# Kernel optimization log

Measured on AMD Instinct MI355X. Metric: run time of the kernel, lower is better.

Reference implementation:

```python
import jax, jax.numpy as jnp
import numpy as np

N = 50000      # nodes (B-rep faces)
E = 800000     # directed edges (avg degree 16)
F_IN = 9       # 8 surface-type flags + is_feature
H1, H2, C = 512, 128, 2


def setup_inputs() -> dict:
    key = jax.random.key(0)
    ks = jax.random.split(key, 8)
    x = jax.random.normal(ks[0], (N, F_IN), dtype=jnp.float32)
    edge_index = jax.random.randint(ks[1], (2, E), 0, N, dtype=jnp.int64)
    W1 = jax.random.normal(ks[2], (F_IN, H1), dtype=jnp.float32) / np.sqrt(F_IN)
    b1 = jnp.zeros((H1,), dtype=jnp.float32)
    W2 = jax.random.normal(ks[3], (H1, H2), dtype=jnp.float32) / np.sqrt(H1)
    b2 = jnp.zeros((H2,), dtype=jnp.float32)
    W3 = jax.random.normal(ks[4], (H2, C), dtype=jnp.float32) / np.sqrt(H2)
    b3 = jnp.zeros((C,), dtype=jnp.float32)
    return {"x": x, "W1": W1, "b1": b1, "W2": W2, "b2": b2,
            "W3": W3, "b3": b3, "edge_index": edge_index}


def reference(x, W1, b1, W2, b2, W3, b3, edge_index):
    n = x.shape[0]
    self_idx = jnp.arange(n, dtype=edge_index.dtype)
    # GCN with self-loops and symmetric normalization (PyG gcn_norm)
    src = jnp.concatenate([edge_index[0], self_idx])  # [E+N]
    dst = jnp.concatenate([edge_index[1], self_idx])  # [E+N]
    deg = jax.ops.segment_sum(jnp.ones_like(src, dtype=x.dtype), dst, num_segments=n)
    dinv = jnp.where(deg > 0, jax.lax.rsqrt(jnp.maximum(deg, 1.0)), 0.0)
    norm = dinv[src] * dinv[dst]  # [E+N]

    def gcn(h, W, b):
        h = h @ W                                   # [N, out]
        msg = h[src] * norm[:, None]                # gather + scale
        return jax.ops.segment_sum(msg, dst, num_segments=n) + b  # scatter-add

    h = jax.nn.relu(gcn(x, W1, b1))
    h = jax.nn.relu(gcn(h, W2, b2))
    # F.dropout with training=False is identity (inference mode)
    h = gcn(h, W3, b3)
    return jax.nn.log_softmax(h, axis=1)
```

## Files before the change

### kernel.cpp

```cpp
#include <hip/hip_runtime.h>
#include <hip/hip_bf16.h>

typedef __attribute__((ext_vector_type(8))) short short8;
typedef __attribute__((ext_vector_type(4))) float float4v;
typedef unsigned int uint;

#define NBLK 192

static __device__ __forceinline__ float2 up_bf2(uint v) {
    float2 r;
    r.x = __uint_as_float(v << 16);
    r.y = __uint_as_float(v & 0xffff0000u);
    return r;
}
static __device__ __forceinline__ short f2bf_bits(float x) {
    union { __hip_bfloat16 h; short s; } u;
    u.h = __float2bfloat16(x);
    return u.s;
}


__global__ __launch_bounds__(256) void k_hist(const int* __restrict__ dst, int E, int chunk,
        int shift, int nbuck, int* __restrict__ histBlk) {
    __shared__ int h[256];
    h[threadIdx.x] = 0;
    __syncthreads();
    int blk = blockIdx.x;
    int e0 = blk * chunk, e1 = min(E, e0 + chunk);
    for (int e = e0 + threadIdx.x; e < e1; e += 256)
        atomicAdd(&h[dst[e] >> shift], 1);
    __syncthreads();
    if (threadIdx.x < nbuck) histBlk[threadIdx.x * NBLK + blk] = h[threadIdx.x];
}


__global__ __launch_bounds__(256) void k_btot(const int* __restrict__ histBlk,
                                              int* __restrict__ btot) {
    __shared__ int s[256];
    int b = blockIdx.x, t = threadIdx.x;
    s[t] = (t < NBLK) ? histBlk[b * NBLK + t] : 0;
    __syncthreads();
    for (int off = 128; off; off >>= 1) {
        if (t < off) s[t] += s[t + off];
        __syncthreads();
    }
    if (t == 0) btot[b] = s[0];
}


__global__ __launch_bounds__(256) void k_bscan(const int* __restrict__ histBlk,
        const int* __restrict__ btot, int nbuck,
        int* __restrict__ baseBlk, int* __restrict__ bucketBase) {
    __shared__ int s[256], sb[256];
    int b = blockIdx.x, t = threadIdx.x;
    int v = (t < NBLK) ? histBlk[b * NBLK + t] : 0;
    s[t] = v;
    sb[t] = (t < nbuck) ? btot[t] : 0;
    __syncthreads();
    for (int off = 1; off < 256; off <<= 1) {
        int u = (t >= off) ? s[t - off] : 0;
        int u2 = (t >= off) ? sb[t - off] : 0;
        __syncthreads();
        s[t] += u;
        sb[t] += u2;
        __syncthreads();
    }
    int base = (b > 0) ? sb[b - 1] : 0;
    if (t < NBLK) baseBlk[b * NBLK + t] = base + s[t] - v;
    if (t == 0) bucketBase[b] = base;
}


__global__ __launch_bounds__(256) void k_scatterbin(const int* __restrict__ src,
        const int* __restrict__ dst, int E, int chunk, int shift, int nbuck,
        const int* __restrict__ baseBlk, uint* __restrict__ binned) {
    __shared__ int cur[256];
    int blk = blockIdx.x;
    if (threadIdx.x < nbuck) cur[threadIdx.x] = baseBlk[threadIdx.x * NBLK + blk];
    __syncthreads();
    int e0 = blk * chunk, e1 = min(E, e0 + chunk);
    int mask = (1 << shift) - 1;
    for (int e = e0 + threadIdx.x; e < e1; e += 256) {
        int d = dst[e];
        int pos = atomicAdd(&cur[d >> shift], 1);
        binned[pos] = (uint)src[e] | ((uint)(d & mask) << 24);
    }
}


__global__ __launch_bounds__(256) void k_csrbuild(const uint* __restrict__ binned,
        const int* __restrict__ bucketBase, const float* __restrict__ x,
        int E, int shift, int n, int nbuck,
        int* __restrict__ row_ptr, float* __restrict__ dinv, float* __restrict__ xs,
        int* __restrict__ csr) {
    __shared__ int cnt[256], lcur[256];
    int b = blockIdx.x, t = threadIdx.x;
    cnt[t] = 0;
    __syncthreads();
    int lo = bucketBase[b];
    int hi = (b + 1 < nbuck) ? bucketBase[b + 1] : E;
    for (int e = lo + t; e < hi; e += 256)
        atomicAdd(&cnt[binned[e] >> 24], 1);
    __syncthreads();
    int c = cnt[t];
    lcur[t] = c;
    __syncthreads();
    for (int off = 1; off < 256; off <<= 1) {
        int u = (t >= off) ? lcur[t - off] : 0;
        __syncthreads();
        lcur[t] += u;
        __syncthreads();
    }
    int node0 = b << shift;
    int nodeEnd = min(n, (b + 1) << shift);
    int cntNodes = nodeEnd - node0;
    int myBase = lo + lcur[t] - c;
    if (t < cntNodes) {
        row_ptr[node0 + t] = myBase;
        dinv[node0 + t] = rsqrtf((float)(c + 1));
    }
    if (b == nbuck - 1 && t == 0) row_ptr[n] = E;
    for (int j = t; j < cntNodes * 9; j += 256) {
        int nl = j / 9, f = j - nl * 9;
        float dnl = rsqrtf((float)(cnt[nl] + 1));
        xs[(size_t)(node0 + nl) * 9 + f] = dnl * x[(size_t)(node0 + nl) * 9 + f];
    }
    __syncthreads();
    lcur[t] = myBase;
    __syncthreads();
    for (int e = lo + t; e < hi; e += 256) {
        uint p = binned[e];
        int pos = atomicAdd(&lcur[p >> 24], 1);
        csr[pos] = (int)(p & 0xFFFFFF);
    }
}


__global__ __launch_bounds__(256) void k_agg1w(const float* __restrict__ xs,
                       const float* __restrict__ dinv,
                       const int* __restrict__ row_ptr, const int* __restrict__ csr,
                       const float* __restrict__ W1, const float* __restrict__ W2,
                       __hip_bfloat16* __restrict__ aggx_bf,
                       __hip_bfloat16* __restrict__ W1frag,
                       __hip_bfloat16* __restrict__ W2frag, int n, int nagg) {
    int bid = blockIdx.x;
    if (bid >= nagg) {
        int xb = bid - nagg;
        if (xb < 8) {
            int t = xb * 256 + threadIdx.x;
            if (t < 32 * 64) {
                int ctile = t >> 6, lane = t & 63;
                int col = ctile * 16 + (lane & 15);
                int k0 = (lane >> 4) * 8;
                short8 o;
#pragma unroll
                for (int j = 0; j < 8; ++j) {
                    int k = k0 + j;
                    o[j] = f2bf_bits(k < 9 ? W1[k * 512 + col] : 0.f);
                }
                *reinterpret_cast<short8*>(W1frag + (size_t)t * 8) = o;
            }
        } else {
            int t = (xb - 8) * 256 + threadIdx.x;
            if (t < 64 * 128) {
                int kb = t >> 7, c = t & 127;
                const float* wp = W2 + (size_t)(kb * 8) * 128 + c;
                short8 o;
#pragma unroll
                for (int j = 0; j < 8; ++j) o[j] = f2bf_bits(wp[j * 128]);
                *reinterpret_cast<short8*>(W2frag + (size_t)t * 8) = o;
            }
        }
        return;
    }
    int node = bid * 16 + (threadIdx.x >> 4);
    if (node >= n) return;
    int f = threadIdx.x & 15;
    bool act = f < 9;
    float acc = act ? xs[node * 9 + f] : 0.f;
    int e0 = row_ptr[node], e1 = row_ptr[node + 1];
    int e = e0;
    for (; e + 4 <= e1; e += 4) {
        int s0 = csr[e], s1 = csr[e + 1], s2 = csr[e + 2], s3 = csr[e + 3];
        float x0 = act ? xs[s0 * 9 + f] : 0.f;
        float x1 = act ? xs[s1 * 9 + f] : 0.f;
        float x2 = act ? xs[s2 * 9 + f] : 0.f;
        float x3 = act ? xs[s3 * 9 + f] : 0.f;
        acc += (x0 + x1) + (x2 + x3);
    }
    for (; e < e1; ++e) {
        int sA = csr[e];
        acc += act ? xs[sA * 9 + f] : 0.f;
    }
    float v = act ? dinv[node] * acc : 0.f;
    __hip_bfloat16* op = aggx_bf + (size_t)node * 32;
    union { __hip_bfloat16 h; short s; } u;
    u.h = __float2bfloat16(v);
    reinterpret_cast<short*>(op)[f] = u.s;
    reinterpret_cast<short*>(op)[16 + f] = 0;
}

__global__ __launch_bounds__(512, 2) void k_l12(const __hip_bfloat16* __restrict__ aggx_bf,
                       const __hip_bfloat16* __restrict__ W1frag,
                       const __hip_bfloat16* __restrict__ W2frag,
                       const float* __restrict__ b1,
                       const float* __restrict__ dinv,
                       __hip_bfloat16* __restrict__ t2, int n, int npair) {
    __shared__ short h1s[8][2][16][40];
    int t = threadIdx.x;
    int wid = t >> 6, lane = t & 63;
    int pair = blockIdx.x * 8 + wid;
    if (pair >= npair) return;
    int r = lane & 15, quad = lane >> 4;
    short (*hs0)[40] = h1s[wid][0];
    short (*hs1)[40] = h1s[wid][1];

    int m0 = pair << 5;
    short8 aagg0 = *reinterpret_cast<const short8*>(
        aggx_bf + (size_t)(m0 + r) * 32 + quad * 8);
    short8 aagg1 = *reinterpret_cast<const short8*>(
        aggx_bf + (size_t)(m0 + 16 + r) * 32 + quad * 8);

    float4v acc0[8], acc1[8];
#pragma unroll
    for (int cg = 0; cg < 8; ++cg) {
        acc0[cg] = (float4v){0, 0, 0, 0};
        acc1[cg] = (float4v){0, 0, 0, 0};
    }

    for (int kt = 0; kt < 16; ++kt) {
        short8 bf0 = *reinterpret_cast<const short8*>(
            W1frag + ((size_t)(2 * kt) * 64 + lane) * 8);
        short8 bf1 = *reinterpret_cast<const short8*>(
            W1frag + ((size_t)(2 * kt + 1) * 64 + lane) * 8);
        float4v c00 = __builtin_amdgcn_mfma_f32_16x16x32_bf16(
            aagg0, bf0, (float4v){0, 0, 0, 0}, 0, 0, 0);
        float4v c01 = __builtin_amdgcn_mfma_f32_16x16x32_bf16(
            aagg0, bf1, (float4v){0, 0, 0, 0}, 0, 0, 0);
        float4v c10 = __builtin_amdgcn_mfma_f32_16x16x32_bf16(
            aagg1, bf0, (float4v){0, 0, 0, 0}, 0, 0, 0);
        float4v c11 = __builtin_amdgcn_mfma_f32_16x16x32_bf16(
            aagg1, bf1, (float4v){0, 0, 0, 0}, 0, 0, 0);
        float bb0 = b1[kt * 32 + r];
        float bb1 = b1[kt * 32 + 16 + r];
        short8 bfr[8];
#pragma unroll
        for (int cg = 0; cg < 8; ++cg)
            bfr[cg] = *reinterpret_cast<const short8*>(
                W2frag + (size_t)(((kt * 4 + quad) * 128) + cg * 16 + r) * 8);
#pragma unroll
        for (int i = 0; i < 4; ++i) {
            int row = quad * 4 + i;
            hs0[row][r]      = f2bf_bits(fmaxf(c00[i] + bb0, 0.f));
            hs0[row][16 + r] = f2bf_bits(fmaxf(c01[i] + bb1, 0.f));
            hs1[row][r]      = f2bf_bits(fmaxf(c10[i] + bb0, 0.f));
            hs1[row][16 + r] = f2bf_bits(fmaxf(c11[i] + bb1, 0.f));
        }
        short8 am0 = *reinterpret_cast<const short8*>(&hs0[r][quad * 8]);
        short8 am1 = *reinterpret_cast<const short8*>(&hs1[r][quad * 8]);
#pragma unroll
        for (int cg = 0; cg < 8; ++cg) {
            acc0[cg] = __builtin_amdgcn_mfma_f32_16x16x32_bf16(am0, bfr[cg], acc0[cg], 0, 0, 0);
            acc1[cg] = __builtin_amdgcn_mfma_f32_16x16x32_bf16(am1, bfr[cg], acc1[cg], 0, 0, 0);
        }
    }

#pragma unroll
    for (int i = 0; i < 4; ++i) {
        int node0 = m0 + quad * 4 + i;
        if (node0 < n) {
            float di = dinv[node0];
            __hip_bfloat16* op = t2 + (size_t)node0 * 128 + r;
#pragma unroll
            for (int cg = 0; cg < 8; ++cg)
                op[cg * 16] = __float2bfloat16(di * acc0[cg][i]);
        }
        int node1 = m0 + 16 + quad * 4 + i;
        if (node1 < n) {
            float di = dinv[node1];
            __hip_bfloat16* op = t2 + (size_t)node1 * 128 + r;
#pragma unroll
            for (int cg = 0; cg < 8; ++cg)
                op[cg * 16] = __float2bfloat16(di * acc1[cg][i]);
        }
    }
}


__global__ __launch_bounds__(256) void k_agg2(const uint* __restrict__ t2u,
                       const float* __restrict__ dinv,
                       const int* __restrict__ row_ptr, const int* __restrict__ csr,
                       const float* __restrict__ b2, const float* __restrict__ W3,
                       float2* __restrict__ t3, int n) {
    int node = blockIdx.x * 4 + (threadIdx.x >> 6);
    if (node >= n) return;
    int lane = threadIdx.x & 63;
    int half = lane >> 5;
    int cl = lane & 31;
    const uint2* t2v = reinterpret_cast<const uint2*>(t2u);

    float a0 = 0.f, a1 = 0.f, a2 = 0.f, a3 = 0.f;
    if (half == 0) {
        uint2 sv = t2v[(size_t)node * 32 + cl];
        float2 pa = up_bf2(sv.x), pb = up_bf2(sv.y);
        a0 = pa.x; a1 = pa.y; a2 = pb.x; a3 = pb.y;
    }

    int e0 = row_ptr[node], e1 = row_ptr[node + 1];
    int eb = e0;
    for (; eb + 16 <= e1; eb += 16) {
        int si[8];
        uint2 ri[8];
#pragma unroll
        for (int j = 0; j < 8; ++j) si[j] = csr[eb + half + 2 * j];
#pragma unroll
        for (int j = 0; j < 8; ++j) ri[j] = t2v[(size_t)si[j] * 32 + cl];
#pragma unroll
        for (int j = 0; j < 8; ++j) {
            float2 qa = up_bf2(ri[j].x), qb = up_bf2(ri[j].y);
            a0 += qa.x; a1 += qa.y; a2 += qb.x; a3 += qb.y;
        }
    }
    for (; eb + 4 <= e1; eb += 4) {
        int s0 = csr[eb + half], s1 = csr[eb + half + 2];
        uint2 r0 = t2v[(size_t)s0 * 32 + cl];
        uint2 r1 = t2v[(size_t)s1 * 32 + cl];
        float2 qa = up_bf2(r0.x), qb = up_bf2(r0.y);
        float2 qc = up_bf2(r1.x), qd = up_bf2(r1.y);
        a0 += qa.x + qc.x; a1 += qa.y + qc.y;
        a2 += qb.x + qd.x; a3 += qb.y + qd.y;
    }
    for (int e = eb + half; e < e1; e += 2) {
        uint2 rv = t2v[(size_t)csr[e] * 32 + cl];
        float2 qa = up_bf2(rv.x), qb = up_bf2(rv.y);
        a0 += qa.x; a1 += qa.y; a2 += qb.x; a3 += qb.y;
    }

    a0 += __shfl_xor(a0, 32);
    a1 += __shfl_xor(a1, 32);
    a2 += __shfl_xor(a2, 32);
    a3 += __shfl_xor(a3, 32);

    float di = dinv[node];
    float4 bb = *reinterpret_cast<const float4*>(b2 + 4 * cl);
    float h0 = fmaxf(di * a0 + bb.x, 0.f);
    float h1v = fmaxf(di * a1 + bb.y, 0.f);
    float h2 = fmaxf(di * a2 + bb.z, 0.f);
    float h3 = fmaxf(di * a3 + bb.w, 0.f);
    float4 wlo = *reinterpret_cast<const float4*>(W3 + 8 * cl);
    float4 whi = *reinterpret_cast<const float4*>(W3 + 8 * cl + 4);
    float c0 = h0 * wlo.x + h1v * wlo.z + h2 * whi.x + h3 * whi.z;
    float c1 = h0 * wlo.y + h1v * wlo.w + h2 * whi.y + h3 * whi.w;
#pragma unroll
    for (int off = 16; off; off >>= 1) {
        c0 += __shfl_xor(c0, off);
        c1 += __shfl_xor(c1, off);
    }
    if (lane == 0) t3[node] = make_float2(di * c0, di * c1);
}


__global__ void k_agg3(const float2* __restrict__ t3, const float* __restrict__ dinv,
                       const int* __restrict__ row_ptr, const int* __restrict__ csr,
                       const float* __restrict__ b3, float2* __restrict__ outv, int n) {
    int node = blockIdx.x * blockDim.x + threadIdx.x;
    if (node >= n) return;
    float2 s = t3[node];
    float a0 = s.x, a1 = s.y;
    int e0 = row_ptr[node], e1 = row_ptr[node + 1];
    int e = e0;
    for (; e + 4 <= e1; e += 4) {
        int s0 = csr[e], s1 = csr[e + 1], s2 = csr[e + 2], s3 = csr[e + 3];
        float2 q0 = t3[s0], q1 = t3[s1], q2 = t3[s2], q3 = t3[s3];
        a0 += q0.x + q1.x + q2.x + q3.x;
        a1 += q0.y + q1.y + q2.y + q3.y;
    }
    for (; e < e1; ++e) {
        float2 q0 = t3[csr[e]];
        a0 += q0.x;
        a1 += q0.y;
    }
    float di = dinv[node];
    float z0 = di * a0 + b3[0];
    float z1 = di * a1 + b3[1];
    float m = fmaxf(z0, z1);
    float lse = m + logf(expf(z0 - m) + expf(z1 - m));
    outv[node] = make_float2(z0 - lse, z1 - lse);
}


extern "C" void kernel_launch(void* const* d_in, const int* in_sizes, int n_in,
                              void* d_out, int out_size, void* d_ws, size_t ws_size,
                              hipStream_t stream) {
    const float* x  = (const float*)d_in[0];
    const float* W1 = (const float*)d_in[1];
    const float* b1 = (const float*)d_in[2];
    const float* W2 = (const float*)d_in[3];
    const float* b2 = (const float*)d_in[4];
    const float* W3 = (const float*)d_in[5];
    const float* b3 = (const float*)d_in[6];
    const int* edges = (const int*)d_in[7];

    int n = in_sizes[0] / 9;
    int E = in_sizes[7] / 2;
    const int* src = edges;
    const int* dst = edges + E;

    char* p = (char*)d_ws;
    auto alloc = [&](size_t bytes) {
        char* q = p;
        p += (bytes + 511) & ~(size_t)511;
        return q;
    };
    float* dinv       = (float*)alloc((size_t)n * 4);
    int*   row_ptr    = (int*)alloc((size_t)(n + 1) * 4);
    int*   csr        = (int*)alloc((size_t)E * 4);
    int*   histBlk    = (int*)alloc((size_t)256 * NBLK * 4);
    int*   baseBlk    = (int*)alloc((size_t)256 * NBLK * 4);
    int*   btot       = (int*)alloc(256 * 4);
    int*   bucketBase = (int*)alloc(256 * 4);
    uint*  binned     = (uint*)alloc((size_t)E * 4);
    float* xs         = (float*)alloc((size_t)n * 9 * 4);
    __hip_bfloat16* aggx_bf = (__hip_bfloat16*)alloc((size_t)(n + 64) * 32 * 2);
    __hip_bfloat16* W1frag  = (__hip_bfloat16*)alloc((size_t)32 * 64 * 8 * 2);
    __hip_bfloat16* W2frag  = (__hip_bfloat16*)alloc((size_t)64 * 128 * 8 * 2);
    __hip_bfloat16* t2 = (__hip_bfloat16*)alloc((size_t)n * 128 * 2);
    float2* t3 = (float2*)alloc((size_t)n * 8);

    const int B = 256;
    int shift = 8;
    int nbuck = ((n - 1) >> shift) + 1;
    int chunk = (E + NBLK - 1) / NBLK;

    k_hist<<<NBLK, B, 0, stream>>>(dst, E, chunk, shift, nbuck, histBlk);
    k_btot<<<nbuck, B, 0, stream>>>(histBlk, btot);
    k_bscan<<<nbuck, B, 0, stream>>>(histBlk, btot, nbuck, baseBlk, bucketBase);
    k_scatterbin<<<NBLK, B, 0, stream>>>(src, dst, E, chunk, shift, nbuck, baseBlk, binned);
    k_csrbuild<<<nbuck, B, 0, stream>>>(binned, bucketBase, x, E, shift, n, nbuck,
                                        row_ptr, dinv, xs, csr);

    int nagg = (n + 15) / 16;
    k_agg1w<<<nagg + 40, B, 0, stream>>>(xs, dinv, row_ptr, csr, W1, W2,
                                         aggx_bf, W1frag, W2frag, n, nagg);

    int ntile = (n + 15) / 16;
    int npair = (ntile + 1) / 2;
    k_l12<<<(npair + 7) / 8, 512, 0, stream>>>(aggx_bf, W1frag, W2frag, b1, dinv, t2, n, npair);
    k_agg2<<<(n + 3) / 4, 256, 0, stream>>>((const uint*)t2, dinv, row_ptr, csr, b2, W3, t3, n);

    k_agg3<<<(n + B - 1) / B, B, 0, stream>>>(t3, dinv, row_ptr, csr, b3, (float2*)d_out, n);
}
```

Before: 196.3 us.

## Replace two-pass bucketed CSR build with global-atomic degree count and fill

Replaces the five-kernel bucket-sort CSR construction (histogram, bucket totals, scan, scatter to binned, per-bucket local sort) with a global atomic per-node degree count, a per-256-node scan, and a fill pass using global atomic cursors. The intermediate binned array and its second pass are removed, and the W1/W2 fragment prep moves into the degree kernel. This trades launches and memory passes for heavy global atomic traffic on random node addresses, and neighbor order within a row becomes nondeterministic. A memset is added to zero the degree and bucket arrays.

```diff
diff --git a/kernel.cpp b/kernel.cpp
--- a/kernel.cpp
+++ b/kernel.cpp
@@ -20,132 +20,13 @@
 }
 
 
-__global__ __launch_bounds__(256) void k_hist(const int* __restrict__ dst, int E, int chunk,
-        int shift, int nbuck, int* __restrict__ histBlk) {
-    __shared__ int h[256];
-    h[threadIdx.x] = 0;
-    __syncthreads();
+__global__ __launch_bounds__(256) void k_deg(const int* __restrict__ dst, int E, int chunk,
+        int nbuck, int nblk, int* __restrict__ deg, int* __restrict__ btot,
+        const float* __restrict__ W1, const float* __restrict__ W2,
+        __hip_bfloat16* __restrict__ W1frag, __hip_bfloat16* __restrict__ W2frag) {
     int blk = blockIdx.x;
-    int e0 = blk * chunk, e1 = min(E, e0 + chunk);
-    for (int e = e0 + threadIdx.x; e < e1; e += 256)
-        atomicAdd(&h[dst[e] >> shift], 1);
-    __syncthreads();
-    if (threadIdx.x < nbuck) histBlk[threadIdx.x * NBLK + blk] = h[threadIdx.x];
-}
-
-
-__global__ __launch_bounds__(256) void k_btot(const int* __restrict__ histBlk,
-                                              int* __restrict__ btot) {
-    __shared__ int s[256];
-    int b = blockIdx.x, t = threadIdx.x;
-    s[t] = (t < NBLK) ? histBlk[b * NBLK + t] : 0;
-    __syncthreads();
-    for (int off = 128; off; off >>= 1) {
-        if (t < off) s[t] += s[t + off];
-        __syncthreads();
-    }
-    if (t == 0) btot[b] = s[0];
-}
-
-
-__global__ __launch_bounds__(256) void k_bscan(const int* __restrict__ histBlk,
-        const int* __restrict__ btot, int nbuck,
-        int* __restrict__ baseBlk, int* __restrict__ bucketBase) {
-    __shared__ int s[256], sb[256];
-    int b = blockIdx.x, t = threadIdx.x;
-    int v = (t < NBLK) ? histBlk[b * NBLK + t] : 0;
-    s[t] = v;
-    sb[t] = (t < nbuck) ? btot[t] : 0;
-    __syncthreads();
-    for (int off = 1; off < 256; off <<= 1) {
-        int u = (t >= off) ? s[t - off] : 0;
-        int u2 = (t >= off) ? sb[t - off] : 0;
-        __syncthreads();
-        s[t] += u;
-        sb[t] += u2;
-        __syncthreads();
-    }
-    int base = (b > 0) ? sb[b - 1] : 0;
-    if (t < NBLK) baseBlk[b * NBLK + t] = base + s[t] - v;
-    if (t == 0) bucketBase[b] = base;
-}
-
-
-__global__ __launch_bounds__(256) void k_scatterbin(const int* __restrict__ src,
-        const int* __restrict__ dst, int E, int chunk, int shift, int nbuck,
-        const int* __restrict__ baseBlk, uint* __restrict__ binned) {
-    __shared__ int cur[256];
-    int blk = blockIdx.x;
-    if (threadIdx.x < nbuck) cur[threadIdx.x] = baseBlk[threadIdx.x * NBLK + blk];
-    __syncthreads();
-    int e0 = blk * chunk, e1 = min(E, e0 + chunk);
-    int mask = (1 << shift) - 1;
-    for (int e = e0 + threadIdx.x; e < e1; e += 256) {
-        int d = dst[e];
-        int pos = atomicAdd(&cur[d >> shift], 1);
-        binned[pos] = (uint)src[e] | ((uint)(d & mask) << 24);
-    }
-}
-
-
-__global__ __launch_bounds__(256) void k_csrbuild(const uint* __restrict__ binned,
-        const int* __restrict__ bucketBase, const float* __restrict__ x,
-        int E, int shift, int n, int nbuck,
-        int* __restrict__ row_ptr, float* __restrict__ dinv, float* __restrict__ xs,
-        int* __restrict__ csr) {
-    __shared__ int cnt[256], lcur[256];
-    int b = blockIdx.x, t = threadIdx.x;
-    cnt[t] = 0;
-    __syncthreads();
-    int lo = bucketBase[b];
-    int hi = (b + 1 < nbuck) ? bucketBase[b + 1] : E;
-    for (int e = lo + t; e < hi; e += 256)
-        atomicAdd(&cnt[binned[e] >> 24], 1);
-    __syncthreads();
-    int c = cnt[t];
-    lcur[t] = c;
-    __syncthreads();
-    for (int off = 1; off < 256; off <<= 1) {
-        int u = (t >= off) ? lcur[t - off] : 0;
-        __syncthreads();
-        lcur[t] += u;
-        __syncthreads();
-    }
-    int node0 = b << shift;
-    int nodeEnd = min(n, (b + 1) << shift);
-    int cntNodes = nodeEnd - node0;
-    int myBase = lo + lcur[t] - c;
-    if (t < cntNodes) {
-        row_ptr[node0 + t] = myBase;
-        dinv[node0 + t] = rsqrtf((float)(c + 1));
-    }
-    if (b == nbuck - 1 && t == 0) row_ptr[n] = E;
-    for (int j = t; j < cntNodes * 9; j += 256) {
-        int nl = j / 9, f = j - nl * 9;
-        float dnl = rsqrtf((float)(cnt[nl] + 1));
-        xs[(size_t)(node0 + nl) * 9 + f] = dnl * x[(size_t)(node0 + nl) * 9 + f];
-    }
-    __syncthreads();
-    lcur[t] = myBase;
-    __syncthreads();
-    for (int e = lo + t; e < hi; e += 256) {
-        uint p = binned[e];
-        int pos = atomicAdd(&lcur[p >> 24], 1);
-        csr[pos] = (int)(p & 0xFFFFFF);
-    }
-}
-
-
-__global__ __launch_bounds__(256) void k_agg1w(const float* __restrict__ xs,
-                       const float* __restrict__ dinv,
-                       const int* __restrict__ row_ptr, const int* __restrict__ csr,
-                       const float* __restrict__ W1, const float* __restrict__ W2,
-                       __hip_bfloat16* __restrict__ aggx_bf,
-                       __hip_bfloat16* __restrict__ W1frag,
-                       __hip_bfloat16* __restrict__ W2frag, int n, int nagg) {
-    int bid = blockIdx.x;
-    if (bid >= nagg) {
-        int xb = bid - nagg;
+    if (blk >= nblk) {
+        int xb = blk - nblk;
         if (xb < 8) {
             int t = xb * 256 + threadIdx.x;
             if (t < 32 * 64) {
@@ -173,7 +54,78 @@
         }
         return;
     }
-    int node = bid * 16 + (threadIdx.x >> 4);
+    __shared__ int h[256];
+    int t = threadIdx.x;
+    h[t] = 0;
+    __syncthreads();
+    int e0 = blk * chunk, e1 = min(E, e0 + chunk);
+    for (int e = e0 + t; e < e1; e += 256) {
+        int d = dst[e];
+        atomicAdd(&deg[d], 1);
+        atomicAdd(&h[d >> 8], 1);
+    }
+    __syncthreads();
+    if (t < nbuck && h[t]) atomicAdd(&btot[t], h[t]);
+}
+
+
+__global__ __launch_bounds__(256) void k_scan(const int* __restrict__ deg,
+        const int* __restrict__ btot, const float* __restrict__ x,
+        int E, int n, int nbuck,
+        int* __restrict__ row_ptr, int* __restrict__ rowcur,
+        float* __restrict__ dinv, float* __restrict__ xs) {
+    __shared__ int s[256], sb[256], cnt[256];
+    int b = blockIdx.x, t = threadIdx.x;
+    int node = (b << 8) + t;
+    int d = (node < n) ? deg[node] : 0;
+    cnt[t] = d;
+    s[t] = d;
+    sb[t] = (t < nbuck) ? btot[t] : 0;
+    __syncthreads();
+    for (int off = 1; off < 256; off <<= 1) {
+        int u = (t >= off) ? s[t - off] : 0;
+        int u2 = (t >= off) ? sb[t - off] : 0;
+        __syncthreads();
+        s[t] += u;
+        sb[t] += u2;
+        __syncthreads();
+    }
+    int base = (b > 0) ? sb[b - 1] : 0;
+    int myBase = base + s[t] - cnt[t];
+    if (node < n) {
+        row_ptr[node] = myBase;
+        rowcur[node] = myBase;
+        dinv[node] = rsqrtf((float)(d + 1));
+    }
+    if (b == nbuck - 1 && t == 0) row_ptr[n] = E;
+    int node0 = b << 8;
+    int cntNodes = min(n, (b + 1) << 8) - node0;
+    for (int j = t; j < cntNodes * 9; j += 256) {
+        int nl = j / 9, f = j - nl * 9;
+        float dnl = rsqrtf((float)(cnt[nl] + 1));
+        xs[(size_t)(node0 + nl) * 9 + f] = dnl * x[(size_t)(node0 + nl) * 9 + f];
+    }
+}
+
+
+__global__ __launch_bounds__(256) void k_fill(const int* __restrict__ src,
+        const int* __restrict__ dst, int E, int chunk,
+        int* __restrict__ rowcur, int* __restrict__ csr) {
+    int blk = blockIdx.x, t = threadIdx.x;
+    int e0 = blk * chunk, e1 = min(E, e0 + chunk);
+    for (int e = e0 + t; e < e1; e += 256) {
+        int d = dst[e];
+        int pos = atomicAdd(&rowcur[d], 1);
+        csr[pos] = src[e];
+    }
+}
+
+
+__global__ __launch_bounds__(256) void k_agg1(const float* __restrict__ xs,
+                       const float* __restrict__ dinv,
+                       const int* __restrict__ row_ptr, const int* __restrict__ csr,
+                       __hip_bfloat16* __restrict__ aggx_bf, int n) {
+    int node = blockIdx.x * 16 + (threadIdx.x >> 4);
     if (node >= n) return;
     int f = threadIdx.x & 15;
     bool act = f < 9;
@@ -414,12 +366,10 @@
     };
     float* dinv       = (float*)alloc((size_t)n * 4);
     int*   row_ptr    = (int*)alloc((size_t)(n + 1) * 4);
+    int*   rowcur     = (int*)alloc((size_t)n * 4);
     int*   csr        = (int*)alloc((size_t)E * 4);
-    int*   histBlk    = (int*)alloc((size_t)256 * NBLK * 4);
-    int*   baseBlk    = (int*)alloc((size_t)256 * NBLK * 4);
-    int*   btot       = (int*)alloc(256 * 4);
-    int*   bucketBase = (int*)alloc(256 * 4);
-    uint*  binned     = (uint*)alloc((size_t)E * 4);
+    int*   deg        = (int*)alloc((size_t)(n + 256) * 4);
+    int*   btot       = deg + n;
     float* xs         = (float*)alloc((size_t)n * 9 * 4);
     __hip_bfloat16* aggx_bf = (__hip_bfloat16*)alloc((size_t)(n + 64) * 32 * 2);
     __hip_bfloat16* W1frag  = (__hip_bfloat16*)alloc((size_t)32 * 64 * 8 * 2);
@@ -428,20 +378,17 @@
     float2* t3 = (float2*)alloc((size_t)n * 8);
 
     const int B = 256;
-    int shift = 8;
-    int nbuck = ((n - 1) >> shift) + 1;
+    int nbuck = ((n - 1) >> 8) + 1;
     int chunk = (E + NBLK - 1) / NBLK;
 
-    k_hist<<<NBLK, B, 0, stream>>>(dst, E, chunk, shift, nbuck, histBlk);
-    k_btot<<<nbuck, B, 0, stream>>>(histBlk, btot);
-    k_bscan<<<nbuck, B, 0, stream>>>(histBlk, btot, nbuck, baseBlk, bucketBase);
-    k_scatterbin<<<NBLK, B, 0, stream>>>(src, dst, E, chunk, shift, nbuck, baseBlk, binned);
-    k_csrbuild<<<nbuck, B, 0, stream>>>(binned, bucketBase, x, E, shift, n, nbuck,
-                                        row_ptr, dinv, xs, csr);
-
-    int nagg = (n + 15) / 16;
-    k_agg1w<<<nagg + 40, B, 0, stream>>>(xs, dinv, row_ptr, csr, W1, W2,
-                                         aggx_bf, W1frag, W2frag, n, nagg);
+    hipMemsetAsync(deg, 0, (size_t)(n + 256) * 4, stream);
+    k_deg<<<NBLK + 40, B, 0, stream>>>(dst, E, chunk, nbuck, NBLK,
+                                       deg, btot, W1, W2, W1frag, W2frag);
+    k_scan<<<nbuck, B, 0, stream>>>(deg, btot, x, E, n, nbuck,
+                                    row_ptr, rowcur, dinv, xs);
+    k_fill<<<NBLK, B, 0, stream>>>(src, dst, E, chunk, rowcur, csr);
+
+    k_agg1<<<(n + 15) / 16, B, 0, stream>>>(xs, dinv, row_ptr, csr, aggx_bf, n);
 
     int ntile = (n + 15) / 16;
     int npair = (ntile + 1) / 2;
```

Result: slower. 243.4 us (+24.0%).

## Split layer-2 aggregation into feature slices with atomic reduction of layer-3 projection

Applied to the files above, without the earlier changes.

Replaces the per-node wavefront aggregation with a kernel where each block handles one of eight 16-feature slices for 32 nodes. Eight threads per node each gather a 4-byte bf16 pair per neighbor, so blocks working on the same slice touch a narrower band of the t2 table, which is meant to improve cache locality. Partial W3 projections from each slice are combined with float atomics into t3, which is now zeroed with a memset beforehand. In exchange, the CSR indices are re-read eight times, each gather is narrower, and the output costs extra atomics.

```diff
diff --git a/kernel.cpp b/kernel.cpp
--- a/kernel.cpp
+++ b/kernel.cpp
@@ -200,6 +200,7 @@
     reinterpret_cast<short*>(op)[16 + f] = 0;
 }
 
+
 __global__ __launch_bounds__(512, 2) void k_l12(const __hip_bfloat16* __restrict__ aggx_bf,
                        const __hip_bfloat16* __restrict__ W1frag,
                        const __hip_bfloat16* __restrict__ W2frag,
@@ -287,76 +288,59 @@
 }
 
 
-__global__ __launch_bounds__(256) void k_agg2(const uint* __restrict__ t2u,
+__global__ __launch_bounds__(256) void k_agg2s(const uint* __restrict__ t2u,
                        const float* __restrict__ dinv,
                        const int* __restrict__ row_ptr, const int* __restrict__ csr,
                        const float* __restrict__ b2, const float* __restrict__ W3,
                        float2* __restrict__ t3, int n) {
-    int node = blockIdx.x * 4 + (threadIdx.x >> 6);
+    int slice = blockIdx.x & 7;
+    int chunk = blockIdx.x >> 3;
+    int t = threadIdx.x;
+    int node = chunk * 32 + (t >> 3);
     if (node >= n) return;
-    int lane = threadIdx.x & 63;
-    int half = lane >> 5;
-    int cl = lane & 31;
-    const uint2* t2v = reinterpret_cast<const uint2*>(t2u);
-
-    float a0 = 0.f, a1 = 0.f, a2 = 0.f, a3 = 0.f;
-    if (half == 0) {
-        uint2 sv = t2v[(size_t)node * 32 + cl];
-        float2 pa = up_bf2(sv.x), pb = up_bf2(sv.y);
-        a0 = pa.x; a1 = pa.y; a2 = pb.x; a3 = pb.y;
-    }
+    int sub = t & 7;
+    int off = slice * 8 + sub;
+
+    float2 p0 = up_bf2(t2u[(size_t)node * 64 + off]);
+    float a0 = p0.x, a1 = p0.y;
 
     int e0 = row_ptr[node], e1 = row_ptr[node + 1];
-    int eb = e0;
-    for (; eb + 16 <= e1; eb += 16) {
+    int e = e0;
+    for (; e + 8 <= e1; e += 8) {
         int si[8];
-        uint2 ri[8];
-#pragma unroll
-        for (int j = 0; j < 8; ++j) si[j] = csr[eb + half + 2 * j];
-#pragma unroll
-        for (int j = 0; j < 8; ++j) ri[j] = t2v[(size_t)si[j] * 32 + cl];
+        uint ri[8];
+#pragma unroll
+        for (int j = 0; j < 8; ++j) si[j] = csr[e + j];
+#pragma unroll
+        for (int j = 0; j < 8; ++j) ri[j] = t2u[(size_t)si[j] * 64 + off];
 #pragma unroll
         for (int j = 0; j < 8; ++j) {
-            float2 qa = up_bf2(ri[j].x), qb = up_bf2(ri[j].y);
-            a0 += qa.x; a1 += qa.y; a2 += qb.x; a3 += qb.y;
-        }
-    }
-    for (; eb + 4 <= e1; eb += 4) {
-        int s0 = csr[eb + half], s1 = csr[eb + half + 2];
-        uint2 r0 = t2v[(size_t)s0 * 32 + cl];
-        uint2 r1 = t2v[(size_t)s1 * 32 + cl];
-        float2 qa = up_bf2(r0.x), qb = up_bf2(r0.y);
-        float2 qc = up_bf2(r1.x), qd = up_bf2(r1.y);
-        a0 += qa.x + qc.x; a1 += qa.y + qc.y;
-        a2 += qb.x + qd.x; a3 += qb.y + qd.y;
-    }
-    for (int e = eb + half; e < e1; e += 2) {
-        uint2 rv = t2v[(size_t)csr[e] * 32 + cl];
-        float2 qa = up_bf2(rv.x), qb = up_bf2(rv.y);
-        a0 += qa.x; a1 += qa.y; a2 += qb.x; a3 += qb.y;
-    }
-
-    a0 += __shfl_xor(a0, 32);
-    a1 += __shfl_xor(a1, 32);
-    a2 += __shfl_xor(a2, 32);
-    a3 += __shfl_xor(a3, 32);
+            float2 q = up_bf2(ri[j]);
+            a0 += q.x;
+            a1 += q.y;
+        }
+    }
+    for (; e < e1; ++e) {
+        float2 q = up_bf2(t2u[(size_t)csr[e] * 64 + off]);
+        a0 += q.x;
+        a1 += q.y;
+    }
 
     float di = dinv[node];
-    float4 bb = *reinterpret_cast<const float4*>(b2 + 4 * cl);
+    int c = off * 2;
+    float2 bb = *reinterpret_cast<const float2*>(b2 + c);
     float h0 = fmaxf(di * a0 + bb.x, 0.f);
-    float h1v = fmaxf(di * a1 + bb.y, 0.f);
-    float h2 = fmaxf(di * a2 + bb.z, 0.f);
-    float h3 = fmaxf(di * a3 + bb.w, 0.f);
-    float4 wlo = *reinterpret_cast<const float4*>(W3 + 8 * cl);
-    float4 whi = *reinterpret_cast<const float4*>(W3 + 8 * cl + 4);
-    float c0 = h0 * wlo.x + h1v * wlo.z + h2 * whi.x + h3 * whi.z;
-    float c1 = h0 * wlo.y + h1v * wlo.w + h2 * whi.y + h3 * whi.w;
-#pragma unroll
-    for (int off = 16; off; off >>= 1) {
-        c0 += __shfl_xor(c0, off);
-        c1 += __shfl_xor(c1, off);
-    }
-    if (lane == 0) t3[node] = make_float2(di * c0, di * c1);
+    float h1 = fmaxf(di * a1 + bb.y, 0.f);
+    float4 wv = *reinterpret_cast<const float4*>(W3 + 2 * c);
+    float c0 = h0 * wv.x + h1 * wv.z;
+    float c1 = h0 * wv.y + h1 * wv.w;
+    c0 += __shfl_xor(c0, 1); c1 += __shfl_xor(c1, 1);
+    c0 += __shfl_xor(c0, 2); c1 += __shfl_xor(c1, 2);
+    c0 += __shfl_xor(c0, 4); c1 += __shfl_xor(c1, 4);
+    if (sub == 0) {
+        atomicAdd(&t3[node].x, di * c0);
+        atomicAdd(&t3[node].y, di * c1);
+    }
 }
 
 
@@ -432,6 +416,8 @@
     int nbuck = ((n - 1) >> shift) + 1;
     int chunk = (E + NBLK - 1) / NBLK;
 
+    hipMemsetAsync(t3, 0, (size_t)n * 8, stream);
+
     k_hist<<<NBLK, B, 0, stream>>>(dst, E, chunk, shift, nbuck, histBlk);
     k_btot<<<nbuck, B, 0, stream>>>(histBlk, btot);
     k_bscan<<<nbuck, B, 0, stream>>>(histBlk, btot, nbuck, baseBlk, bucketBase);
@@ -446,7 +432,9 @@
     int ntile = (n + 15) / 16;
     int npair = (ntile + 1) / 2;
     k_l12<<<(npair + 7) / 8, 512, 0, stream>>>(aggx_bf, W1frag, W2frag, b1, dinv, t2, n, npair);
-    k_agg2<<<(n + 3) / 4, 256, 0, stream>>>((const uint*)t2, dinv, row_ptr, csr, b2, W3, t3, n);
+
+    int nchunk = (n + 31) / 32;
+    k_agg2s<<<nchunk * 8, B, 0, stream>>>((const uint*)t2, dinv, row_ptr, csr, b2, W3, t3, n);
 
     k_agg3<<<(n + B - 1) / B, B, 0, stream>>>(t3, dinv, row_ptr, csr, b3, (float2*)d_out, n);
 }
```

After: 233.7 us. 19.1% more time.
